# Optimization experiments

Measured on AMD Instinct MI355X. Metric: run time of the kernel, lower is better.

Reference implementation:

```python
import jax, jax.numpy as jnp
import numpy as np

B, L, C = 16, 2048, 256
H, R = 6, 32
HEAD_SCALE = 1.0 / np.sqrt(R)


def setup_inputs() -> dict:
    key = jax.random.key(0)
    k1, k2, k3, k4 = jax.random.split(key, 4)
    feats = jax.random.normal(k1, (B, L + 1, C), dtype=jnp.float32)
    Wq = jax.random.normal(k2, (H * R, C), dtype=jnp.float32) * (1.0 / np.sqrt(C))
    Wk = jax.random.normal(k3, (H * R, C), dtype=jnp.float32) * (1.0 / np.sqrt(C))
    Wd = jax.random.normal(k4, (1, C), dtype=jnp.float32) * (1.0 / np.sqrt(C))
    bd = jnp.zeros((1,), dtype=jnp.float32)
    logit_scale = jnp.ones((), dtype=jnp.float32)
    return {"feats": feats, "Wq": Wq, "Wk": Wk, "Wd": Wd, "bd": bd,
            "logit_scale": logit_scale}


def _fold_vertices(feats):
    # drop leading token, pair-average: [B, L+1, C] -> [B, L//2, C]
    x = feats[:, 1:]
    b, l, c = x.shape
    return x.reshape(b, l // 2, 2, c).mean(axis=2)


def reference(feats, Wq, Wk, Wd, bd, logit_scale):
    x = _fold_vertices(feats)                     # [B, N, C]
    b, n, _ = x.shape
    Q = (x @ Wq.T).reshape(b, n, H, R)            # [B, N, H, R]
    K = (x @ Wk.T).reshape(b, n, H, R)
    # sum over heads of per-head low-rank QK^T == contraction over folded (H*R)
    S = jnp.einsum('bnhr,bmhr->bnm', Q, K) * HEAD_SCALE   # [B, N, N]
    d = (x @ Wd.T + bd).squeeze(-1)               # [B, N]
    idx = jnp.arange(n)
    S = S.at[:, idx, idx].add(d)
    return S * jnp.maximum(logit_scale, 0.01)
```

## Files before the change

kernel.cpp:

```cpp
#include <hip/hip_runtime.h>
#include <stdint.h>


#define HD_SCALE 0.17677669529663687f

typedef __bf16 bf16_t;
typedef bf16_t bf16x8 __attribute__((ext_vector_type(8)));
typedef float f32x4 __attribute__((ext_vector_type(4)));

__device__ __forceinline__ unsigned short f2bf(float f) {
  unsigned int u = __float_as_uint(f);
  unsigned int r = (u + 0x7fffu + ((u >> 16) & 1u)) >> 16;
  return (unsigned short)r;
}

__device__ __forceinline__ void gload16(const void* g, void* l) {
  __builtin_amdgcn_global_load_lds(
      (const __attribute__((address_space(1))) void*)g,
      (__attribute__((address_space(3))) void*)l, 16, 0, 0);
}

__global__ __launch_bounds__(256) void k_wconv(const float* __restrict__ Wq,
                                               const float* __restrict__ Wk,
                                               unsigned short* __restrict__ Wqkb) {
  int idx = blockIdx.x * 256 + threadIdx.x;
  float v = (idx < 49152) ? Wq[idx] : Wk[idx - 49152];
  Wqkb[idx] = f2bf(v);
}

__global__ __launch_bounds__(256) void k_fold(const float* __restrict__ feats,
                                              const float* __restrict__ Wd,
                                              const float* __restrict__ bd,
                                              unsigned short* __restrict__ xb,
                                              float* __restrict__ dvec) {
  const int t = threadIdx.x;
  const int wave = t >> 6, lane = t & 63;
  const int gr = blockIdx.x * 4 + wave;
  const int b = gr >> 10, n = gr & 1023;
  const int c = lane * 4;

  const float* r0 = feats + (size_t)(b * 2049 + 1 + 2 * n) * 256 + c;
  float4 p0 = *(const float4*)r0;
  float4 p1 = *(const float4*)(r0 + 256);
  float4 wv = *(const float4*)(Wd + c);

  float x0 = (p0.x + p1.x) * 0.5f;
  float x1 = (p0.y + p1.y) * 0.5f;
  float x2 = (p0.z + p1.z) * 0.5f;
  float x3 = (p0.w + p1.w) * 0.5f;

  ushort4 xs;
  xs.x = f2bf(x0); xs.y = f2bf(x1); xs.z = f2bf(x2); xs.w = f2bf(x3);
  *(ushort4*)&xb[(size_t)gr * 256 + c] = xs;

  float dot = x0 * wv.x + x1 * wv.y + x2 * wv.z + x3 * wv.w;
#pragma unroll
  for (int o = 32; o > 0; o >>= 1) dot += __shfl_down(dot, o, 64);
  if (lane == 0) dvec[gr] = dot + bd[0];
}

__global__ __launch_bounds__(256) void k_proj(const unsigned short* __restrict__ xb,
                                              const unsigned short* __restrict__ Wqkb,
                                              unsigned short* __restrict__ QK) {
  __shared__ unsigned short As[128 * 32];
  __shared__ unsigned short Bs[128 * 32];
  const int t = threadIdx.x;
  const int w = t >> 6, l = t & 63;
  const int m0 = blockIdx.x * 128;
  const int n0 = blockIdx.y * 128;
  const int wm = w >> 1, wn = w & 1;
  const int quad = l >> 4, lr = l & 15;

  f32x4 acc[4][4];
#pragma unroll
  for (int i = 0; i < 4; ++i)
#pragma unroll
    for (int j = 0; j < 4; ++j) acc[i][j] = (f32x4){0.f, 0.f, 0.f, 0.f};

  for (int kk = 0; kk < 8; ++kk) {
    const int k0 = kk * 32;
    __syncthreads();
#pragma unroll
    for (int i = 0; i < 2; ++i) {
      const int e = w * 128 + i * 64 + l;
      const int row = e >> 2, kc = e & 3;
      gload16(xb + (size_t)(m0 + row) * 256 + k0 + kc * 8,
              &As[(w * 128 + i * 64) * 8]);
      gload16(Wqkb + (size_t)(n0 + row) * 256 + k0 + kc * 8,
              &Bs[(w * 128 + i * 64) * 8]);
    }
    __syncthreads();

    bf16x8 a[4], bfr[4];
#pragma unroll
    for (int i = 0; i < 4; ++i)
      a[i] = *(const bf16x8*)&As[(wm * 64 + i * 16 + lr) * 32 + quad * 8];
#pragma unroll
    for (int j = 0; j < 4; ++j)
      bfr[j] = *(const bf16x8*)&Bs[(wn * 64 + j * 16 + lr) * 32 + quad * 8];
#pragma unroll
    for (int i = 0; i < 4; ++i)
#pragma unroll
      for (int j = 0; j < 4; ++j)
        acc[i][j] = __builtin_amdgcn_mfma_f32_16x16x32_bf16(a[i], bfr[j],
                                                            acc[i][j], 0, 0, 0);
  }

#pragma unroll
  for (int i = 0; i < 4; ++i)
#pragma unroll
    for (int j = 0; j < 4; ++j)
#pragma unroll
      for (int r = 0; r < 4; ++r) {
        const int row = m0 + wm * 64 + i * 16 + quad * 4 + r;
        const int col = n0 + wn * 64 + j * 16 + lr;
        QK[(size_t)row * 384 + col] = f2bf(acc[i][j][r]);
      }
}

__global__ __launch_bounds__(256) void k_score(const unsigned short* __restrict__ QK,
                                               const float* __restrict__ dvec,
                                               const float* __restrict__ logit_scale,
                                               float* __restrict__ out) {
  __shared__ unsigned short As[128 * 32];
  __shared__ unsigned short Bs[128 * 32];
  const int t = threadIdx.x;
  const int w = t >> 6, l = t & 63;
  const int mt = blockIdx.x, nt = blockIdx.y, b = blockIdx.z;
  const int m0 = mt * 128;
  const int n0 = nt * 128;
  const int wm = w >> 1, wn = w & 1;
  const int quad = l >> 4, lr = l & 15;
  const size_t qbase = (size_t)b * 1024 * 384;

  f32x4 acc[4][4];
#pragma unroll
  for (int i = 0; i < 4; ++i)
#pragma unroll
    for (int j = 0; j < 4; ++j) acc[i][j] = (f32x4){0.f, 0.f, 0.f, 0.f};

  for (int kk = 0; kk < 6; ++kk) {
    const int k0 = kk * 32;
    __syncthreads();
#pragma unroll
    for (int i = 0; i < 2; ++i) {
      const int e = w * 128 + i * 64 + l;
      const int row = e >> 2, kc = e & 3;
      gload16(QK + qbase + (size_t)(n0 + row) * 384 + k0 + kc * 8,
              &As[(w * 128 + i * 64) * 8]);
      gload16(QK + qbase + (size_t)(m0 + row) * 384 + 192 + k0 + kc * 8,
              &Bs[(w * 128 + i * 64) * 8]);
    }
    __syncthreads();

    bf16x8 a[4], bfr[4];
#pragma unroll
    for (int i = 0; i < 4; ++i)
      a[i] = *(const bf16x8*)&As[(wm * 64 + i * 16 + lr) * 32 + quad * 8];
#pragma unroll
    for (int j = 0; j < 4; ++j)
      bfr[j] = *(const bf16x8*)&Bs[(wn * 64 + j * 16 + lr) * 32 + quad * 8];
#pragma unroll
    for (int i = 0; i < 4; ++i)
#pragma unroll
      for (int j = 0; j < 4; ++j)
        acc[i][j] = __builtin_amdgcn_mfma_f32_16x16x32_bf16(a[i], bfr[j],
                                                            acc[i][j], 0, 0, 0);
  }

  const float ls = fmaxf(logit_scale[0], 0.01f);
  const bool diag_block = (m0 == n0);
#pragma unroll
  for (int i = 0; i < 4; ++i)
#pragma unroll
    for (int j = 0; j < 4; ++j)
#pragma unroll
      for (int r = 0; r < 4; ++r) {
        const int nr = n0 + wm * 64 + i * 16 + quad * 4 + r;
        const int mc = m0 + wn * 64 + j * 16 + lr;
        float v = acc[i][j][r] * HD_SCALE;
        if (diag_block && nr == mc) v += dvec[b * 1024 + nr];
        out[((size_t)b << 20) + (size_t)nr * 1024 + mc] = v * ls;
      }
}

extern "C" void kernel_launch(void* const* d_in, const int* in_sizes, int n_in,
                              void* d_out, int out_size, void* d_ws, size_t ws_size,
                              hipStream_t stream) {
  const float* feats = (const float*)d_in[0];
  const float* Wq = (const float*)d_in[1];
  const float* Wk = (const float*)d_in[2];
  const float* Wd = (const float*)d_in[3];
  const float* bd = (const float*)d_in[4];
  const float* ls = (const float*)d_in[5];
  float* out = (float*)d_out;

  uint8_t* ws = (uint8_t*)d_ws;
  unsigned short* xb = (unsigned short*)ws;
  unsigned short* QK = (unsigned short*)(ws + (8u << 20));
  float* dvec = (float*)(ws + (20u << 20));
  unsigned short* Wqkb = (unsigned short*)(ws + (20u << 20) + (64u << 10));

  hipLaunchKernelGGL(k_wconv, dim3(384), dim3(256), 0, stream, Wq, Wk, Wqkb);
  hipLaunchKernelGGL(k_fold, dim3(4096), dim3(256), 0, stream, feats, Wd, bd, xb, dvec);
  hipLaunchKernelGGL(k_proj, dim3(128, 3), dim3(256), 0, stream, xb, Wqkb, QK);
  hipLaunchKernelGGL(k_score, dim3(8, 8, 16), dim3(256), 0, stream, QK, dvec, ls, out);
}
```

Baseline: 128.2 us.

## Merge prep kernels, deepen K tiles with XOR-swizzled LDS, nontemporal output stores

Fuses the weight-conversion and fold kernels into one launch to cut a kernel launch. In both GEMM kernels, the K step doubles from 32 to 64 and the LDS layout gets an XOR swizzle, which halves the barrier/load iterations and reduces LDS bank conflicts. The score kernel writes its 64MB output with nontemporal stores to avoid cache pollution. LDS use per block doubles, which can reduce occupancy.

```diff
diff --git a/kernel.cpp b/kernel.cpp
--- a/kernel.cpp
+++ b/kernel.cpp
@@ -10,8 +10,7 @@
 
 __device__ __forceinline__ unsigned short f2bf(float f) {
   unsigned int u = __float_as_uint(f);
-  unsigned int r = (u + 0x7fffu + ((u >> 16) & 1u)) >> 16;
-  return (unsigned short)r;
+  return (unsigned short)((u + 0x7fffu + ((u >> 16) & 1u)) >> 16);
 }
 
 __device__ __forceinline__ void gload16(const void* g, void* l) {
@@ -20,20 +19,20 @@
       (__attribute__((address_space(3))) void*)l, 16, 0, 0);
 }
 
-__global__ __launch_bounds__(256) void k_wconv(const float* __restrict__ Wq,
-                                               const float* __restrict__ Wk,
-                                               unsigned short* __restrict__ Wqkb) {
-  int idx = blockIdx.x * 256 + threadIdx.x;
-  float v = (idx < 49152) ? Wq[idx] : Wk[idx - 49152];
-  Wqkb[idx] = f2bf(v);
-}
-
-__global__ __launch_bounds__(256) void k_fold(const float* __restrict__ feats,
+__global__ __launch_bounds__(256) void k_prep(const float* __restrict__ feats,
+                                              const float* __restrict__ Wq,
+                                              const float* __restrict__ Wk,
                                               const float* __restrict__ Wd,
                                               const float* __restrict__ bd,
                                               unsigned short* __restrict__ xb,
-                                              float* __restrict__ dvec) {
+                                              float* __restrict__ dvec,
+                                              unsigned short* __restrict__ Wqkb) {
   const int t = threadIdx.x;
+  if (blockIdx.x < 384) {
+    const int idx = blockIdx.x * 256 + t;
+    const float v = (idx < 49152) ? Wq[idx] : Wk[idx - 49152];
+    Wqkb[idx] = f2bf(v);
+  }
   const int wave = t >> 6, lane = t & 63;
   const int gr = blockIdx.x * 4 + wave;
   const int b = gr >> 10, n = gr & 1023;
@@ -62,8 +61,8 @@
 __global__ __launch_bounds__(256) void k_proj(const unsigned short* __restrict__ xb,
                                               const unsigned short* __restrict__ Wqkb,
                                               unsigned short* __restrict__ QK) {
-  __shared__ unsigned short As[128 * 32];
-  __shared__ unsigned short Bs[128 * 32];
+  __shared__ unsigned short As[128 * 64];
+  __shared__ unsigned short Bs[128 * 64];
   const int t = threadIdx.x;
   const int w = t >> 6, l = t & 63;
   const int m0 = blockIdx.x * 128;
@@ -71,39 +70,45 @@
   const int wm = w >> 1, wn = w & 1;
   const int quad = l >> 4, lr = l & 15;
 
-  f32x4 acc[4][4];
-#pragma unroll
-  for (int i = 0; i < 4; ++i)
-#pragma unroll
-    for (int j = 0; j < 4; ++j) acc[i][j] = (f32x4){0.f, 0.f, 0.f, 0.f};
-
-  for (int kk = 0; kk < 8; ++kk) {
-    const int k0 = kk * 32;
-    __syncthreads();
-#pragma unroll
-    for (int i = 0; i < 2; ++i) {
-      const int e = w * 128 + i * 64 + l;
-      const int row = e >> 2, kc = e & 3;
+  f32x4 acc[4][4] = {};
+
+  for (int kk = 0; kk < 4; ++kk) {
+    const int k0 = kk * 64;
+    __syncthreads();
+#pragma unroll
+    for (int i = 0; i < 4; ++i) {
+      const int e = i * 256 + t;
+      const int row = e >> 3;
+      const int kc = (e & 7) ^ (row & 7);
       gload16(xb + (size_t)(m0 + row) * 256 + k0 + kc * 8,
-              &As[(w * 128 + i * 64) * 8]);
+              &As[(i * 256 + (w << 6)) * 8]);
       gload16(Wqkb + (size_t)(n0 + row) * 256 + k0 + kc * 8,
-              &Bs[(w * 128 + i * 64) * 8]);
-    }
-    __syncthreads();
-
-    bf16x8 a[4], bfr[4];
-#pragma unroll
-    for (int i = 0; i < 4; ++i)
-      a[i] = *(const bf16x8*)&As[(wm * 64 + i * 16 + lr) * 32 + quad * 8];
-#pragma unroll
-    for (int j = 0; j < 4; ++j)
-      bfr[j] = *(const bf16x8*)&Bs[(wn * 64 + j * 16 + lr) * 32 + quad * 8];
-#pragma unroll
-    for (int i = 0; i < 4; ++i)
-#pragma unroll
-      for (int j = 0; j < 4; ++j)
-        acc[i][j] = __builtin_amdgcn_mfma_f32_16x16x32_bf16(a[i], bfr[j],
-                                                            acc[i][j], 0, 0, 0);
+              &Bs[(i * 256 + (w << 6)) * 8]);
+    }
+    __syncthreads();
+
+#pragma unroll
+    for (int s = 0; s < 2; ++s) {
+      bf16x8 a[4], bb[4];
+#pragma unroll
+      for (int i = 0; i < 4; ++i) {
+        const int row = wm * 64 + i * 16 + lr;
+        const int pos = (s * 4 + quad) ^ (row & 7);
+        a[i] = *(const bf16x8*)&As[row * 64 + pos * 8];
+      }
+#pragma unroll
+      for (int j = 0; j < 4; ++j) {
+        const int row = wn * 64 + j * 16 + lr;
+        const int pos = (s * 4 + quad) ^ (row & 7);
+        bb[j] = *(const bf16x8*)&Bs[row * 64 + pos * 8];
+      }
+#pragma unroll
+      for (int i = 0; i < 4; ++i)
+#pragma unroll
+        for (int j = 0; j < 4; ++j)
+          acc[i][j] = __builtin_amdgcn_mfma_f32_16x16x32_bf16(a[i], bb[j],
+                                                              acc[i][j], 0, 0, 0);
+    }
   }
 
 #pragma unroll
@@ -122,8 +127,8 @@
                                                const float* __restrict__ dvec,
                                                const float* __restrict__ logit_scale,
                                                float* __restrict__ out) {
-  __shared__ unsigned short As[128 * 32];
-  __shared__ unsigned short Bs[128 * 32];
+  __shared__ unsigned short As[128 * 64];
+  __shared__ unsigned short Bs[128 * 64];
   const int t = threadIdx.x;
   const int w = t >> 6, l = t & 63;
   const int mt = blockIdx.x, nt = blockIdx.y, b = blockIdx.z;
@@ -133,39 +138,45 @@
   const int quad = l >> 4, lr = l & 15;
   const size_t qbase = (size_t)b * 1024 * 384;
 
-  f32x4 acc[4][4];
-#pragma unroll
-  for (int i = 0; i < 4; ++i)
-#pragma unroll
-    for (int j = 0; j < 4; ++j) acc[i][j] = (f32x4){0.f, 0.f, 0.f, 0.f};
-
-  for (int kk = 0; kk < 6; ++kk) {
-    const int k0 = kk * 32;
-    __syncthreads();
-#pragma unroll
-    for (int i = 0; i < 2; ++i) {
-      const int e = w * 128 + i * 64 + l;
-      const int row = e >> 2, kc = e & 3;
+  f32x4 acc[4][4] = {};
+
+  for (int kk = 0; kk < 3; ++kk) {
+    const int k0 = kk * 64;
+    __syncthreads();
+#pragma unroll
+    for (int i = 0; i < 4; ++i) {
+      const int e = i * 256 + t;
+      const int row = e >> 3;
+      const int kc = (e & 7) ^ (row & 7);
       gload16(QK + qbase + (size_t)(n0 + row) * 384 + k0 + kc * 8,
-              &As[(w * 128 + i * 64) * 8]);
+              &As[(i * 256 + (w << 6)) * 8]);
       gload16(QK + qbase + (size_t)(m0 + row) * 384 + 192 + k0 + kc * 8,
-              &Bs[(w * 128 + i * 64) * 8]);
-    }
-    __syncthreads();
-
-    bf16x8 a[4], bfr[4];
-#pragma unroll
-    for (int i = 0; i < 4; ++i)
-      a[i] = *(const bf16x8*)&As[(wm * 64 + i * 16 + lr) * 32 + quad * 8];
-#pragma unroll
-    for (int j = 0; j < 4; ++j)
-      bfr[j] = *(const bf16x8*)&Bs[(wn * 64 + j * 16 + lr) * 32 + quad * 8];
-#pragma unroll
-    for (int i = 0; i < 4; ++i)
-#pragma unroll
-      for (int j = 0; j < 4; ++j)
-        acc[i][j] = __builtin_amdgcn_mfma_f32_16x16x32_bf16(a[i], bfr[j],
-                                                            acc[i][j], 0, 0, 0);
+              &Bs[(i * 256 + (w << 6)) * 8]);
+    }
+    __syncthreads();
+
+#pragma unroll
+    for (int s = 0; s < 2; ++s) {
+      bf16x8 a[4], bb[4];
+#pragma unroll
+      for (int i = 0; i < 4; ++i) {
+        const int row = wm * 64 + i * 16 + lr;
+        const int pos = (s * 4 + quad) ^ (row & 7);
+        a[i] = *(const bf16x8*)&As[row * 64 + pos * 8];
+      }
+#pragma unroll
+      for (int j = 0; j < 4; ++j) {
+        const int row = wn * 64 + j * 16 + lr;
+        const int pos = (s * 4 + quad) ^ (row & 7);
+        bb[j] = *(const bf16x8*)&Bs[row * 64 + pos * 8];
+      }
+#pragma unroll
+      for (int i = 0; i < 4; ++i)
+#pragma unroll
+        for (int j = 0; j < 4; ++j)
+          acc[i][j] = __builtin_amdgcn_mfma_f32_16x16x32_bf16(a[i], bb[j],
+                                                              acc[i][j], 0, 0, 0);
+    }
   }
 
   const float ls = fmaxf(logit_scale[0], 0.01f);
@@ -180,7 +191,8 @@
         const int mc = m0 + wn * 64 + j * 16 + lr;
         float v = acc[i][j][r] * HD_SCALE;
         if (diag_block && nr == mc) v += dvec[b * 1024 + nr];
-        out[((size_t)b << 20) + (size_t)nr * 1024 + mc] = v * ls;
+        __builtin_nontemporal_store(v * ls,
+            &out[((size_t)b << 20) + (size_t)nr * 1024 + mc]);
       }
 }
 
@@ -201,8 +213,8 @@
   float* dvec = (float*)(ws + (20u << 20));
   unsigned short* Wqkb = (unsigned short*)(ws + (20u << 20) + (64u << 10));
 
-  hipLaunchKernelGGL(k_wconv, dim3(384), dim3(256), 0, stream, Wq, Wk, Wqkb);
-  hipLaunchKernelGGL(k_fold, dim3(4096), dim3(256), 0, stream, feats, Wd, bd, xb, dvec);
+  hipLaunchKernelGGL(k_prep, dim3(4096), dim3(256), 0, stream, feats, Wq, Wk, Wd, bd,
+                     xb, dvec, Wqkb);
   hipLaunchKernelGGL(k_proj, dim3(128, 3), dim3(256), 0, stream, xb, Wqkb, QK);
   hipLaunchKernelGGL(k_score, dim3(8, 8, 16), dim3(256), 0, stream, QK, dvec, ls, out);
 }
```

Result: no change. 127.2 us (-0.8%).
